# Optimization experiments

Hardware: AMD Instinct MI355X
Metric: run time of the kernel (lower is better)

## Reference

```python
import jax, jax.numpy as jnp
import numpy as np

N = 500_000   # nodes
E = 16_000_000  # edges
G = 5_000     # graphs
H = 64        # hidden_channels
BN_EPS = 1e-5


def setup_inputs() -> dict:
    key = jax.random.key(0)
    ks = jax.random.split(key, 8)
    f32 = jnp.float32
    return {
        "x": jax.random.normal(ks[0], (N, 4), f32),
        "eps": jnp.zeros((), f32),
        "w1": jax.random.normal(ks[1], (4, 2 * H), f32) * 0.5,
        "b1": jnp.zeros((2 * H,), f32),
        "g1": jnp.ones((2 * H,), f32),
        "be1": jnp.zeros((2 * H,), f32),
        "m1": jnp.zeros((2 * H,), f32),
        "v1": jnp.ones((2 * H,), f32),
        "w2": jax.random.normal(ks[2], (2 * H, H), f32) * 0.1,
        "b2": jnp.zeros((H,), f32),
        "g2": jnp.ones((H,), f32),
        "be2": jnp.zeros((H,), f32),
        "m2": jnp.zeros((H,), f32),
        "v2": jnp.ones((H,), f32),
        "w3": jax.random.normal(ks[3], (H, 2), f32) * 0.1,
        "b3": jnp.zeros((2,), f32),
        "edge_index": jax.random.randint(ks[4], (2, E), 0, N, dtype=jnp.int64) if jax.config.jax_enable_x64 else jax.random.randint(ks[4], (2, E), 0, N, dtype=jnp.int32),
        "batch": jnp.sort(jax.random.randint(ks[5], (N,), 0, G, dtype=jnp.int32)),
    }


def _bn_eval(h, g, be, m, v):
    # BatchNorm1d in eval mode: affine transform with running stats
    return (h - m) * (g * jax.lax.rsqrt(v + BN_EPS)) + be


def reference(x, eps, w1, b1, g1, be1, m1, v1, w2, b2, g2, be2, m2, v2,
              w3, b3, edge_index, batch):
    src, dst = edge_index[0], edge_index[1]
    # GINConv: h_i = nn((1+eps)*x_i + sum_{j->i} x_j)   (adj_t @ x)
    agg = jax.ops.segment_sum(x[src], dst, num_segments=N)  # [N,4]
    h = (1.0 + eps) * x + agg
    # MLP: Linear-BN-ReLU-Linear-BN-ReLU
    h = jax.nn.relu(_bn_eval(h @ w1 + b1, g1, be1, m1, v1))   # [N,128]
    h = jax.nn.relu(_bn_eval(h @ w2 + b2, g2, be2, m2, v2))   # [N,64]
    # dropout is identity at inference
    # global_mean_pool over graphs
    sums = jax.ops.segment_sum(h, batch, num_segments=G)      # [G,64]
    cnt = jax.ops.segment_sum(jnp.ones((N, 1), h.dtype), batch, num_segments=G)
    pooled = sums / jnp.maximum(cnt, 1.0)
    logits = pooled @ w3 + b3                                 # [G,2]
    return jax.nn.log_softmax(logits, axis=-1)
```

## Files before the change

### kernel.cpp

```cpp
#include <hip/hip_runtime.h>
#include <hip/hip_fp16.h>

#define N_NODES  500000
#define N_EDGES  16000000
#define N_GRAPHS 5000

#define NBIN  512
#define BSZN  1024
#define CH    8192
#define NCH   1954

#define FXS   262144.0f
#define FXI   3.814697265625e-06f

#define WS_AGG     0
#define WS_SUMS    2000000
#define WS_CNT     2320000
#define WS_W1F     2325008
#define WS_B1F     2325520
#define WS_W2F     2325648
#define WS_B2F     2333840
#define WS_HIST    2333904
#define WS_XH      WS_HIST
#define WS_BTOT    3334352
#define WS_BSTART  3334864
#define WS_CSR     3335380
#define WS_TOTAL_ELEMS 19335380

typedef __attribute__((ext_vector_type(8))) short short8;
typedef __attribute__((ext_vector_type(4))) float f32x4;
typedef __attribute__((ext_vector_type(4))) unsigned int u32x4;

static __device__ __forceinline__ unsigned short bf16r(float f) {
    unsigned int u = __float_as_uint(f);
    u = u + 0x7FFFu + ((u >> 16) & 1u);
    return (unsigned short)(u >> 16);
}

__global__ void k_prep(const float* __restrict__ w1, const float* __restrict__ b1,
                       const float* __restrict__ g1, const float* __restrict__ be1,
                       const float* __restrict__ m1, const float* __restrict__ v1,
                       const float* __restrict__ w2, const float* __restrict__ b2,
                       const float* __restrict__ g2, const float* __restrict__ be2,
                       const float* __restrict__ m2, const float* __restrict__ v2,
                       float* __restrict__ ws) {
    int t = threadIdx.x;
    if (t < 128) {
        float s = g1[t] * rsqrtf(v1[t] + 1e-5f);
        ws[WS_B1F + t] = (b1[t] - m1[t]) * s + be1[t];
        for (int c = 0; c < 4; ++c)
            ws[WS_W1F + t * 4 + c] = w1[c * 128 + t] * s;
    }
    if (t < 64) {
        float s = g2[t] * rsqrtf(v2[t] + 1e-5f);
        ws[WS_B2F + t] = (b2[t] - m2[t]) * s + be2[t];
        unsigned short* w2t = (unsigned short*)(ws + WS_W2F);
        for (int j = 0; j < 128; ++j)
            w2t[t * 128 + j] = bf16r(w2[j * 64 + t] * s);
    }
}

__global__ __launch_bounds__(256) void k_xhalf(const float4* __restrict__ x4,
                                               uint2* __restrict__ xh) {
    int i = blockIdx.x * 256 + threadIdx.x;
    if (i >= N_NODES) return;
    float4 v = x4[i];
    __half2 a = __floats2half2_rn(v.x, v.y);
    __half2 b = __floats2half2_rn(v.z, v.w);
    uint2 p;
    p.x = *(unsigned int*)&a;
    p.y = *(unsigned int*)&b;
    xh[i] = p;
}

__global__ __launch_bounds__(256) void k_e1_hist(const int* __restrict__ ei,
                                                 int* __restrict__ hist) {
    __shared__ int h[NBIN];
    int t = threadIdx.x, blk = blockIdx.x;
    for (int i = t; i < NBIN; i += 256) h[i] = 0;
    __syncthreads();
    int base = blk * CH;
    int nE = min(CH, N_EDGES - base);
    const int4* d4 = (const int4*)(ei + N_EDGES + base);
    for (int i = t; i < (nE >> 2); i += 256) {
        int4 d = d4[i];
        atomicAdd(&h[d.x >> 10], 1);
        atomicAdd(&h[d.y >> 10], 1);
        atomicAdd(&h[d.z >> 10], 1);
        atomicAdd(&h[d.w >> 10], 1);
    }
    __syncthreads();
    for (int i = t; i < NBIN; i += 256) hist[blk * NBIN + i] = h[i];
}

__global__ __launch_bounds__(256) void k_e2a_scan(int* __restrict__ hist,
                                                  int* __restrict__ binTotal) {
    __shared__ int buf[2048];
    __shared__ int wsum[4], woff2[4];
    int t = threadIdx.x, bin = blockIdx.x;
    for (int i = t; i < 2048; i += 256)
        buf[i] = (i < NCH) ? hist[i * NBIN + bin] : 0;
    __syncthreads();
    int s = 0;
    #pragma unroll
    for (int k = 0; k < 8; ++k) s += buf[t * 8 + k];
    int inc = s;
    #pragma unroll
    for (int dlt = 1; dlt < 64; dlt <<= 1) {
        int n = __shfl_up(inc, dlt, 64);
        if ((t & 63) >= dlt) inc += n;
    }
    if ((t & 63) == 63) wsum[t >> 6] = inc;
    __syncthreads();
    if (t == 0) { int r = 0; for (int w = 0; w < 4; ++w) { woff2[w] = r; r += wsum[w]; } }
    __syncthreads();
    int run = inc - s + woff2[t >> 6];
    #pragma unroll
    for (int k = 0; k < 8; ++k) { int v = buf[t * 8 + k]; buf[t * 8 + k] = run; run += v; }
    __syncthreads();
    if (t == 0) binTotal[bin] = woff2[3] + wsum[3];
    for (int i = t; i < NCH; i += 256) hist[i * NBIN + bin] = buf[i];
}

__global__ __launch_bounds__(512) void k_e2b_scan(const int* __restrict__ binTotal,
                                                  int* __restrict__ binStart) {
    __shared__ int wtot[8], woff[8];
    int t = threadIdx.x;
    int v = binTotal[t];
    int inc = v;
    #pragma unroll
    for (int dlt = 1; dlt < 64; dlt <<= 1) {
        int n = __shfl_up(inc, dlt, 64);
        if ((t & 63) >= dlt) inc += n;
    }
    if ((t & 63) == 63) wtot[t >> 6] = inc;
    __syncthreads();
    if (t == 0) { int r = 0; for (int w = 0; w < 8; ++w) { woff[w] = r; r += wtot[w]; } }
    __syncthreads();
    int excl = inc - v + woff[t >> 6];
    binStart[t] = excl;
    if (t == NBIN - 1) binStart[NBIN] = excl + v;
}

#define E3T 512
__global__ __launch_bounds__(E3T) void k_e3_sort(const int* __restrict__ ei,
                                                 const int* __restrict__ hist,
                                                 const int* __restrict__ binStart,
                                                 unsigned int* __restrict__ csr) {
    __shared__ unsigned int ebuf[CH];
    __shared__ int lhist[NBIN];
    __shared__ int gbase[NBIN];
    __shared__ int cursor[NBIN];
    __shared__ int wtot[8], woff[8];
    int t = threadIdx.x, c = blockIdx.x;

    lhist[t] = 0;
    __syncthreads();

    int base = c * CH;
    int nE = min(CH, N_EDGES - base);
    {
        const int4* d4 = (const int4*)(ei + N_EDGES + base);
        for (int i = t; i < (nE >> 2); i += E3T) {
            int4 d = d4[i];
            atomicAdd(&lhist[d.x >> 10], 1);
            atomicAdd(&lhist[d.y >> 10], 1);
            atomicAdd(&lhist[d.z >> 10], 1);
            atomicAdd(&lhist[d.w >> 10], 1);
        }
    }
    __syncthreads();
    int v = lhist[t];
    int inc = v;
    #pragma unroll
    for (int dlt = 1; dlt < 64; dlt <<= 1) {
        int n = __shfl_up(inc, dlt, 64);
        if ((t & 63) >= dlt) inc += n;
    }
    if ((t & 63) == 63) wtot[t >> 6] = inc;
    __syncthreads();
    if (t == 0) { int r = 0; for (int w = 0; w < 8; ++w) { woff[w] = r; r += wtot[w]; } }
    __syncthreads();
    int excl = inc - v + woff[t >> 6];
    cursor[t] = excl;
    gbase[t]  = binStart[t] + hist[c * NBIN + t];
    __syncthreads();
    {
        const int4* s4 = (const int4*)(ei + base);
        const int4* d4 = (const int4*)(ei + N_EDGES + base);
        for (int i = t; i < (nE >> 2); i += E3T) {
            int4 s = s4[i];
            int4 d = d4[i];
            int p0 = atomicAdd(&cursor[d.x >> 10], 1);
            ebuf[p0] = ((unsigned int)s.x << 10) | (unsigned int)(d.x & 1023);
            int p1 = atomicAdd(&cursor[d.y >> 10], 1);
            ebuf[p1] = ((unsigned int)s.y << 10) | (unsigned int)(d.y & 1023);
            int p2 = atomicAdd(&cursor[d.z >> 10], 1);
            ebuf[p2] = ((unsigned int)s.z << 10) | (unsigned int)(d.z & 1023);
            int p3 = atomicAdd(&cursor[d.w >> 10], 1);
            ebuf[p3] = ((unsigned int)s.w << 10) | (unsigned int)(d.w & 1023);
        }
    }
    __syncthreads();
    int grp = t >> 4, lane = t & 15;
    for (int b = grp; b < NBIN; b += (E3T / 16)) {
        int n  = lhist[b];
        int lb = cursor[b] - n;
        int gb = gbase[b];
        for (int j = lane; j < n; j += 16)
            csr[gb + j] = ebuf[lb + j];
    }
}

__global__ __launch_bounds__(1024) void k_e4_agg(const unsigned int* __restrict__ csr,
                                                 const int* __restrict__ binStart,
                                                 const uint2* __restrict__ xh,
                                                 int* __restrict__ aggi) {
    __shared__ int aggs_i[BSZN * 4];
    int t = threadIdx.x;
    int bin  = blockIdx.x >> 1;
    int half = blockIdx.x & 1;
    for (int i = t; i < BSZN * 4; i += 1024) aggs_i[i] = 0;
    __syncthreads();
    int s0 = binStart[bin];
    int e0 = binStart[bin + 1];
    int mid = s0 + ((e0 - s0) >> 1);
    int start = half ? mid : s0;
    int end   = half ? e0  : mid;

#define E4_PROC(vv) {                                              \
        unsigned int v_ = (vv);                                    \
        int src_ = (int)(v_ >> 10);                                \
        int loc_ = (int)(v_ & 1023u);                              \
        uint2 p_ = xh[src_];                                       \
        __half2 ab_ = *(__half2*)&p_.x;                            \
        __half2 cd_ = *(__half2*)&p_.y;                            \
        float2 f0_ = __half22float2(ab_);                          \
        float2 f1_ = __half22float2(cd_);                          \
        atomicAdd(&aggs_i[0 * BSZN + loc_], __float2int_rn(f0_.x * FXS)); \
        atomicAdd(&aggs_i[1 * BSZN + loc_], __float2int_rn(f0_.y * FXS)); \
        atomicAdd(&aggs_i[2 * BSZN + loc_], __float2int_rn(f1_.x * FXS)); \
        atomicAdd(&aggs_i[3 * BSZN + loc_], __float2int_rn(f1_.y * FXS)); \
    }

    int as = (start + 3) & ~3; if (as > end) as = end;
    int ae = end & ~3;         if (ae < as)  ae = as;
    if (t < (as - start)) E4_PROC(csr[start + t]);
    if (t < (end - ae))   E4_PROC(csr[ae + t]);
    const u32x4* c4 = (const u32x4*)csr;
    for (int i = (as >> 2) + t; i < (ae >> 2); i += 1024) {
        u32x4 v = __builtin_nontemporal_load(&c4[i]);
        E4_PROC(v.x); E4_PROC(v.y); E4_PROC(v.z); E4_PROC(v.w);
    }
#undef E4_PROC

    __syncthreads();
    int nodeBase = bin * BSZN;
    if (nodeBase >= N_NODES) return;
    int nv = min(BSZN, N_NODES - nodeBase) * 4;
    for (int i = t; i < nv; i += 1024) {
        int pv = aggs_i[(i & 3) * BSZN + (i >> 2)];
        if (pv) atomicAdd(&aggi[nodeBase * 4 + i], pv);
    }
}

__global__ __launch_bounds__(256) void k_edge(const int* __restrict__ ei,
                                              const float4* __restrict__ x4,
                                              float* __restrict__ aggf) {
    int e = blockIdx.x * 256 + threadIdx.x;
    if (e >= N_EDGES) return;
    int s = ei[e];
    int d = ei[N_EDGES + e];
    float4 v = x4[s];
    atomicAdd(&aggf[d * 4 + 0], v.x);
    atomicAdd(&aggf[d * 4 + 1], v.y);
    atomicAdd(&aggf[d * 4 + 2], v.z);
    atomicAdd(&aggf[d * 4 + 3], v.w);
}

__global__ __launch_bounds__(512) void k_node(const float4* __restrict__ x4,
                                              const int* __restrict__ aggi,
                                              const float* __restrict__ aggf,
                                              int useFix,
                                              const int* __restrict__ batch,
                                              const float* __restrict__ epsp,
                                              const float* __restrict__ ws,
                                              float* __restrict__ sums,
                                              float* __restrict__ cnt) {
    __shared__ float w1s4[4 * 516];
    __shared__ float b1s[128];
    __shared__ float b2s[64];
    __shared__ float h2t[8][16][68];
    __shared__ int   bshW[128];

    int tid  = threadIdx.x;
    int wave = tid >> 6;
    int l    = tid & 63;
    int cl   = l & 15;
    int q8   = l >> 4;

    for (int i = tid; i < 2048; i += 512)
        w1s4[(i >> 9) * 516 + (i & 511)] = ws[WS_W1F + (i & 511)];
    if (tid < 128) b1s[tid] = ws[WS_B1F + tid];
    if (tid < 64)  b2s[tid] = ws[WS_B2F + tid];

    const unsigned short* w2t = (const unsigned short*)(ws + WS_W2F);
    short8 bfr[4][4];
    #pragma unroll
    for (int nt = 0; nt < 4; ++nt)
        #pragma unroll
        for (int ks = 0; ks < 4; ++ks)
            bfr[nt][ks] = *(const short8*)(w2t + (nt * 16 + cl) * 128 + ks * 32 + q8 * 8);

    __syncthreads();

    int tilebase = blockIdx.x * 128 + wave * 16;
    int node = tilebase + cl;
    bool valid = node < N_NODES;
    float4 xi = valid ? x4[node] : make_float4(0.f, 0.f, 0.f, 0.f);
    float4 ai;
    if (valid) {
        if (useFix) {
            int4 av = ((const int4*)aggi)[node];
            ai = make_float4(av.x * FXI, av.y * FXI, av.z * FXI, av.w * FXI);
        } else {
            ai = ((const float4*)aggf)[node];
        }
    } else ai = make_float4(0.f, 0.f, 0.f, 0.f);
    int bn = valid ? batch[node] : -1;
    if (l < 16) bshW[wave * 16 + l] = bn;
    float ep = 1.0f + epsp[0];
    float hx = ep * xi.x + ai.x;
    float hy = ep * xi.y + ai.y;
    float hz = ep * xi.z + ai.z;
    float hw = ep * xi.w + ai.w;

    f32x4 acc[4];
    #pragma unroll
    for (int nt = 0; nt < 4; ++nt) acc[nt] = (f32x4){0.f, 0.f, 0.f, 0.f};

    #pragma unroll
    for (int ks = 0; ks < 4; ++ks) {
        short8 afrag;
        #pragma unroll
        for (int e = 0; e < 8; ++e) {
            int j = ks * 32 + q8 * 8 + e;
            const float4 wr = *(const float4*)&w1s4[q8 * 516 + j * 4];
            float h1 = fmaf(hx, wr.x, fmaf(hy, wr.y, fmaf(hz, wr.z, fmaf(hw, wr.w, b1s[j]))));
            h1 = fmaxf(h1, 0.0f);
            afrag[e] = (short)bf16r(h1);
        }
        #pragma unroll
        for (int nt = 0; nt < 4; ++nt)
            acc[nt] = __builtin_amdgcn_mfma_f32_16x16x32_bf16(afrag, bfr[nt][ks], acc[nt], 0, 0, 0);
    }

    float h2v[4][4];
    #pragma unroll
    for (int nt = 0; nt < 4; ++nt) {
        float b2v = b2s[nt * 16 + cl];
        #pragma unroll
        for (int r = 0; r < 4; ++r)
            h2v[nt][r] = fmaxf(acc[nt][r] + b2v, 0.0f);
    }

    int firstb = __shfl(bn, 0);
    bool uni = __all(bn == firstb) && (firstb >= 0);
    if (uni) {
        float s[4];
        #pragma unroll
        for (int nt = 0; nt < 4; ++nt) {
            float v = h2v[nt][0] + h2v[nt][1] + h2v[nt][2] + h2v[nt][3];
            v += __shfl_xor(v, 16);
            v += __shfl_xor(v, 32);
            s[nt] = v;
        }
        if (l < 16) {
            #pragma unroll
            for (int nt = 0; nt < 4; ++nt)
                atomicAdd(&sums[firstb * 64 + nt * 16 + l], s[nt]);
        }
        if (l == 0) atomicAdd(&cnt[firstb], 16.0f);
    } else {
        #pragma unroll
        for (int nt = 0; nt < 4; ++nt)
            #pragma unroll
            for (int r = 0; r < 4; ++r)
                h2t[wave][q8 * 4 + r][nt * 16 + cl] = h2v[nt][r];
        int kout = l;
        float a = 0.f, c = 0.f;
        int cur = -1;
        for (int n = 0; n < 16; ++n) {
            int bn2 = bshW[wave * 16 + n];
            if (bn2 != cur) {
                if (cur >= 0) {
                    atomicAdd(&sums[cur * 64 + kout], a);
                    if (l == 0) atomicAdd(&cnt[cur], c);
                }
                a = 0.f; c = 0.f; cur = bn2;
            }
            if (bn2 >= 0) { a += h2t[wave][n][kout]; c += 1.f; }
        }
        if (cur >= 0) {
            atomicAdd(&sums[cur * 64 + kout], a);
            if (l == 0) atomicAdd(&cnt[cur], c);
        }
    }
}

__global__ __launch_bounds__(256) void k_head(const float* __restrict__ sums,
                                              const float* __restrict__ cnt,
                                              const float* __restrict__ w3,
                                              const float* __restrict__ b3,
                                              float* __restrict__ out) {
    int g = blockIdx.x * 256 + threadIdx.x;
    if (g >= N_GRAPHS) return;
    float ic = 1.0f / fmaxf(cnt[g], 1.0f);
    float l0 = b3[0], l1 = b3[1];
    #pragma unroll 8
    for (int k = 0; k < 64; ++k) {
        float p = sums[g * 64 + k] * ic;
        l0 = fmaf(p, w3[k * 2 + 0], l0);
        l1 = fmaf(p, w3[k * 2 + 1], l1);
    }
    float m = fmaxf(l0, l1);
    float lse = m + logf(expf(l0 - m) + expf(l1 - m));
    out[g * 2 + 0] = l0 - lse;
    out[g * 2 + 1] = l1 - lse;
}

extern "C" void kernel_launch(void* const* d_in, const int* in_sizes, int n_in,
                              void* d_out, int out_size, void* d_ws, size_t ws_size,
                              hipStream_t stream) {
    const float* x   = (const float*)d_in[0];
    const float* eps = (const float*)d_in[1];
    const float* w1  = (const float*)d_in[2];
    const float* b1  = (const float*)d_in[3];
    const float* g1  = (const float*)d_in[4];
    const float* be1 = (const float*)d_in[5];
    const float* m1  = (const float*)d_in[6];
    const float* v1  = (const float*)d_in[7];
    const float* w2  = (const float*)d_in[8];
    const float* b2  = (const float*)d_in[9];
    const float* g2  = (const float*)d_in[10];
    const float* be2 = (const float*)d_in[11];
    const float* m2  = (const float*)d_in[12];
    const float* v2  = (const float*)d_in[13];
    const float* w3  = (const float*)d_in[14];
    const float* b3  = (const float*)d_in[15];
    const int*   ei  = (const int*)d_in[16];
    const int*   batch = (const int*)d_in[17];

    float* ws = (float*)d_ws;
    int*   wsi = (int*)d_ws;

    k_prep<<<1, 128, 0, stream>>>(w1, b1, g1, be1, m1, v1, w2, b2, g2, be2, m2, v2, ws);

    if (ws_size >= (size_t)WS_TOTAL_ELEMS * 4) {
        (void)hipMemsetAsync(ws, 0, (size_t)2325000 * sizeof(float), stream);

        k_e1_hist<<<NCH, 256, 0, stream>>>(ei, wsi + WS_HIST);
        k_e2a_scan<<<NBIN, 256, 0, stream>>>(wsi + WS_HIST, wsi + WS_BTOT);
        k_e2b_scan<<<1, NBIN, 0, stream>>>(wsi + WS_BTOT, wsi + WS_BSTART);
        k_e3_sort<<<NCH, E3T, 0, stream>>>(ei, wsi + WS_HIST, wsi + WS_BSTART,
                                           (unsigned int*)(wsi + WS_CSR));
        k_xhalf<<<(N_NODES + 255) / 256, 256, 0, stream>>>((const float4*)x,
                                                           (uint2*)(wsi + WS_XH));
        k_e4_agg<<<NBIN * 2, 1024, 0, stream>>>((const unsigned int*)(wsi + WS_CSR),
                                                wsi + WS_BSTART,
                                                (const uint2*)(wsi + WS_XH),
                                                wsi + WS_AGG);
        k_node<<<(N_NODES + 127) / 128, 512, 0, stream>>>(
            (const float4*)x, wsi + WS_AGG, (const float*)nullptr, 1, batch, eps, ws,
            ws + WS_SUMS, ws + WS_CNT);
    } else {
        (void)hipMemsetAsync(ws + WS_SUMS, 0, (size_t)325000 * sizeof(float), stream);
        (void)hipMemsetAsync(ws + WS_CSR, 0, (size_t)2000000 * sizeof(float), stream);
        k_edge<<<(N_EDGES + 255) / 256, 256, 0, stream>>>(ei, (const float4*)x,
                                                          ws + WS_CSR);
        k_node<<<(N_NODES + 127) / 128, 512, 0, stream>>>(
            (const float4*)x, (const int*)nullptr, ws + WS_CSR, 0, batch, eps, ws,
            ws + WS_SUMS, ws + WS_CNT);
    }

    k_head<<<(N_GRAPHS + 255) / 256, 256, 0, stream>>>(
        ws + WS_SUMS, ws + WS_CNT, w3, b3, (float*)d_out);
}
```

Measured before the change: 271.3 us.

## Reuse scanned histogram in sort, drop agg halves and agg memset

The sort kernel now derives each chunk's per-bin counts from the exclusive-scanned histogram (next row minus current, or the bin total for the last chunk) instead of re-reading the destination indices and rebuilding a shared-memory histogram. The aggregation kernel goes back to one block per bin, so it can write results directly with plain stores instead of global atomics, which also removes the memset of the 2M-entry aggregation buffer. The trade-off is half as many aggregation blocks (512 blocks of 1024 threads), which reduces parallelism in the gather phase. Correctness depends on the histogram buffer holding a column-wise exclusive scan after k_e2a_scan.

New measurement: 261.6 us. -3.6%, faster.

```diff
diff --git a/kernel.cpp b/kernel.cpp
--- a/kernel.cpp
+++ b/kernel.cpp
@@ -145,6 +145,7 @@
 #define E3T 512
 __global__ __launch_bounds__(E3T) void k_e3_sort(const int* __restrict__ ei,
                                                  const int* __restrict__ hist,
+                                                 const int* __restrict__ binTotal,
                                                  const int* __restrict__ binStart,
                                                  unsigned int* __restrict__ csr) {
     __shared__ unsigned int ebuf[CH];
@@ -154,23 +155,13 @@
     __shared__ int wtot[8], woff[8];
     int t = threadIdx.x, c = blockIdx.x;
 
-    lhist[t] = 0;
-    __syncthreads();
-
     int base = c * CH;
     int nE = min(CH, N_EDGES - base);
-    {
-        const int4* d4 = (const int4*)(ei + N_EDGES + base);
-        for (int i = t; i < (nE >> 2); i += E3T) {
-            int4 d = d4[i];
-            atomicAdd(&lhist[d.x >> 10], 1);
-            atomicAdd(&lhist[d.y >> 10], 1);
-            atomicAdd(&lhist[d.z >> 10], 1);
-            atomicAdd(&lhist[d.w >> 10], 1);
-        }
-    }
-    __syncthreads();
-    int v = lhist[t];
+
+    int histcur  = hist[c * NBIN + t];
+    int histnext = (c < NCH - 1) ? hist[(c + 1) * NBIN + t] : binTotal[t];
+    int v = histnext - histcur;
+    lhist[t] = v;
     int inc = v;
     #pragma unroll
     for (int dlt = 1; dlt < 64; dlt <<= 1) {
@@ -183,7 +174,7 @@
     __syncthreads();
     int excl = inc - v + woff[t >> 6];
     cursor[t] = excl;
-    gbase[t]  = binStart[t] + hist[c * NBIN + t];
+    gbase[t]  = binStart[t] + histcur;
     __syncthreads();
     {
         const int4* s4 = (const int4*)(ei + base);
@@ -217,16 +208,11 @@
                                                  const uint2* __restrict__ xh,
                                                  int* __restrict__ aggi) {
     __shared__ int aggs_i[BSZN * 4];
-    int t = threadIdx.x;
-    int bin  = blockIdx.x >> 1;
-    int half = blockIdx.x & 1;
+    int t = threadIdx.x, bin = blockIdx.x;
     for (int i = t; i < BSZN * 4; i += 1024) aggs_i[i] = 0;
     __syncthreads();
-    int s0 = binStart[bin];
-    int e0 = binStart[bin + 1];
-    int mid = s0 + ((e0 - s0) >> 1);
-    int start = half ? mid : s0;
-    int end   = half ? e0  : mid;
+    int start = binStart[bin];
+    int end   = binStart[bin + 1];
 
 #define E4_PROC(vv) {                                              \
         unsigned int v_ = (vv);                                    \
@@ -258,10 +244,8 @@
     int nodeBase = bin * BSZN;
     if (nodeBase >= N_NODES) return;
     int nv = min(BSZN, N_NODES - nodeBase) * 4;
-    for (int i = t; i < nv; i += 1024) {
-        int pv = aggs_i[(i & 3) * BSZN + (i >> 2)];
-        if (pv) atomicAdd(&aggi[nodeBase * 4 + i], pv);
-    }
+    for (int i = t; i < nv; i += 1024)
+        aggi[nodeBase * 4 + i] = aggs_i[(i & 3) * BSZN + (i >> 2)];
 }
 
 __global__ __launch_bounds__(256) void k_edge(const int* __restrict__ ei,
@@ -457,19 +441,20 @@
     k_prep<<<1, 128, 0, stream>>>(w1, b1, g1, be1, m1, v1, w2, b2, g2, be2, m2, v2, ws);
 
     if (ws_size >= (size_t)WS_TOTAL_ELEMS * 4) {
-        (void)hipMemsetAsync(ws, 0, (size_t)2325000 * sizeof(float), stream);
+        (void)hipMemsetAsync(ws + WS_SUMS, 0, (size_t)325000 * sizeof(float), stream);
 
         k_e1_hist<<<NCH, 256, 0, stream>>>(ei, wsi + WS_HIST);
         k_e2a_scan<<<NBIN, 256, 0, stream>>>(wsi + WS_HIST, wsi + WS_BTOT);
         k_e2b_scan<<<1, NBIN, 0, stream>>>(wsi + WS_BTOT, wsi + WS_BSTART);
-        k_e3_sort<<<NCH, E3T, 0, stream>>>(ei, wsi + WS_HIST, wsi + WS_BSTART,
+        k_e3_sort<<<NCH, E3T, 0, stream>>>(ei, wsi + WS_HIST, wsi + WS_BTOT,
+                                           wsi + WS_BSTART,
                                            (unsigned int*)(wsi + WS_CSR));
         k_xhalf<<<(N_NODES + 255) / 256, 256, 0, stream>>>((const float4*)x,
                                                            (uint2*)(wsi + WS_XH));
-        k_e4_agg<<<NBIN * 2, 1024, 0, stream>>>((const unsigned int*)(wsi + WS_CSR),
-                                                wsi + WS_BSTART,
-                                                (const uint2*)(wsi + WS_XH),
-                                                wsi + WS_AGG);
+        k_e4_agg<<<NBIN, 1024, 0, stream>>>((const unsigned int*)(wsi + WS_CSR),
+                                            wsi + WS_BSTART,
+                                            (const uint2*)(wsi + WS_XH),
+                                            wsi + WS_AGG);
         k_node<<<(N_NODES + 127) / 128, 512, 0, stream>>>(
             (const float4*)x, wsi + WS_AGG, (const float*)nullptr, 1, batch, eps, ws,
             ws + WS_SUMS, ws + WS_CNT);
```
